# Kernel tuning notes

Hardware: AMD Instinct MI355X
Metric: run time of the kernel (lower is better)

## Reference

```python
import jax, jax.numpy as jnp
import numpy as np

ALPHA = 0.5
BETA = 5.0
LOGIT_SCALE = 100.0  # exp(log(100)) -- CLIP's learned logit scale at its clamp value
NUM_CLASSES = 200


def _l2norm(x):
    return x / jnp.linalg.norm(x, axis=-1, keepdims=True)


def setup_inputs() -> dict:
    key = jax.random.key(0)
    k1, k2, k3, k4 = jax.random.split(key, 4)
    img_f = jax.random.normal(k1, (1024, 512), dtype=jnp.float32)
    text_features = jax.random.normal(k2, (200, 512), dtype=jnp.float32)
    keys = jax.random.normal(k3, (50000, 512), dtype=jnp.float32)
    labels = jax.random.randint(k4, (50000,), 0, NUM_CLASSES, dtype=jnp.int64)
    return {"img_f": img_f, "text_features": text_features, "keys": keys, "labels": labels}


def reference(img_f, text_features, keys, labels):
    # encode_image output is L2-normalized in the module; keys were built from
    # normalized image features, text_features are normalized class embeddings.
    q = _l2norm(img_f)            # [B, D]
    t = _l2norm(text_features)    # [C, D]
    k = _l2norm(keys)             # [N, D]

    # CLIP zero-shot branch: scale * q @ t.T -> [B, C]
    z = LOGIT_SCALE * jnp.einsum('bd,cd->bc', q, t)

    # Tip-Adapter cache branch: exp(beta * q @ keys.T) @ one_hot(labels)
    sim = jnp.einsum('bd,nd->bn', q, k)                 # [B, N]
    aff = jnp.exp(BETA * sim)                           # [B, N]
    values = jax.nn.one_hot(labels, NUM_CLASSES, dtype=aff.dtype)  # [N, C]
    c = aff @ values                                    # [B, C]

    return (1.0 - ALPHA) * z + ALPHA * c
```

## Files before the change

kernel.cpp:

```cpp
#include <hip/hip_runtime.h>

#define B_Q    1024
#define D_K    512
#define N_CLS  200
#define N_KEYS 50000
#define N_PAD  50048
#define N_ZT   (N_PAD / 128)

#define R0 N_PAD
#define R1 (R0 + B_Q)
#define R2 (R1 + N_CLS)
#define R3 (R2 + 56)
#define R4 (R3 + 400)

typedef __attribute__((ext_vector_type(8))) short bf16x8;
typedef __attribute__((ext_vector_type(4))) float f32x4;

__device__ __forceinline__ unsigned short f2bf(float f) {
  union { float f; unsigned int i; } v; v.f = f;
  unsigned int r = v.i + 0x7fffu + ((v.i >> 16) & 1u);
  return (unsigned short)(r >> 16);
}
__device__ __forceinline__ uint4 pack8(const float f[8], float s) {
  uint4 o;
  o.x = (unsigned)f2bf(f[0]*s) | ((unsigned)f2bf(f[1]*s) << 16);
  o.y = (unsigned)f2bf(f[2]*s) | ((unsigned)f2bf(f[3]*s) << 16);
  o.z = (unsigned)f2bf(f[4]*s) | ((unsigned)f2bf(f[5]*s) << 16);
  o.w = (unsigned)f2bf(f[6]*s) | ((unsigned)f2bf(f[7]*s) << 16);
  return o;
}
__device__ __forceinline__ void async_copy16(const void* g, void* lds) {
  __builtin_amdgcn_global_load_lds(
      (const __attribute__((address_space(1))) unsigned int*)g,
      (__attribute__((address_space(3))) unsigned int*)lds, 16, 0, 0);
}

__global__ __launch_bounds__(1024) void k_sort(const int* __restrict__ labels,
                                               int* __restrict__ dest) {
  __shared__ int hist[N_CLS];
  __shared__ int incl[N_CLS];
  __shared__ int cur[N_CLS];
  int t = threadIdx.x;
  if (t < N_CLS) hist[t] = 0;
  __syncthreads();
  for (int n = t; n < N_KEYS; n += 1024) atomicAdd(&hist[labels[n]], 1);
  __syncthreads();
  if (t < N_CLS) incl[t] = hist[t];
  __syncthreads();
  for (int d = 1; d < N_CLS; d <<= 1) {
    int x = 0;
    if (t < N_CLS && t >= d) x = incl[t - d];
    __syncthreads();
    if (t < N_CLS) incl[t] += x;
    __syncthreads();
  }
  if (t < N_CLS) cur[t] = incl[t] - hist[t];
  __syncthreads();
  for (int n = t; n < N_KEYS; n += 1024)
    dest[n] = atomicAdd(&cur[labels[n]], 1);
}

__global__ void k_prep2(const float* __restrict__ keys, const float* __restrict__ img,
                        const float* __restrict__ txt, const int* __restrict__ labels,
                        const int* __restrict__ dest, unsigned short* __restrict__ qn,
                        unsigned short* __restrict__ kn, int* __restrict__ cls,
                        float* __restrict__ out) {
  int w = threadIdx.x >> 6, lane = threadIdx.x & 63;
  int row = blockIdx.x * 4 + w;
  const float* src; unsigned short* dst;
  if (row < R0) {
    if (row >= N_KEYS) {
      *((uint4*)(kn + (size_t)row * D_K) + lane) = make_uint4(0, 0, 0, 0);
      if (lane == 0) cls[row] = N_CLS;
      return;
    }
    int d = dest[row];
    if (lane == 0) cls[d] = labels[row];
    src = keys + (size_t)row * D_K;
    dst = kn + (size_t)d * D_K;
  } else if (row < R1) {
    int r = row - R0;
    src = img + (size_t)r * D_K;
    dst = qn + (size_t)r * D_K;
  } else if (row < R2) {
    int r = row - R1;
    if (lane == 0) cls[N_PAD + r] = N_CLS;
    src = txt + (size_t)r * D_K;
    dst = kn + (size_t)(N_PAD + r) * D_K;
  } else if (row < R3) {
    int r = N_PAD + N_CLS + (row - R2);
    *((uint4*)(kn + (size_t)r * D_K) + lane) = make_uint4(0, 0, 0, 0);
    if (lane == 0) cls[r] = N_CLS;
    return;
  } else if (row < R4) {
    int zr = row - R3;
    uint4* o4 = (uint4*)(out + (size_t)zr * 512) + lane * 2;
    o4[0] = make_uint4(0, 0, 0, 0);
    o4[1] = make_uint4(0, 0, 0, 0);
    return;
  } else return;
  const float4* s4 = (const float4*)src + lane * 2;
  float4 a = s4[0], b = s4[1];
  float f[8] = {a.x, a.y, a.z, a.w, b.x, b.y, b.z, b.w};
  float ss = 0.f;
#pragma unroll
  for (int i = 0; i < 8; i++) ss += f[i] * f[i];
#pragma unroll
  for (int d = 1; d < 64; d <<= 1) ss += __shfl_xor(ss, d);
  float rinv = rsqrtf(ss);
  *((uint4*)dst + lane) = pack8(f, rinv);
}

__global__ __launch_bounds__(256, 3) void k_main(const unsigned short* __restrict__ qn,
                                                 const unsigned short* __restrict__ kn,
                                                 const int* __restrict__ cls,
                                                 float* __restrict__ out) {
  __shared__ unsigned short As[128 * 64];
  __shared__ unsigned short Bs[128 * 64];
  int t = threadIdx.x;
  int tileB = blockIdx.x, tileN = blockIdx.y;
  int rowB0 = tileB * 128, rowN0 = tileN * 128;

  f32x4 acc[4][4];
#pragma unroll
  for (int i = 0; i < 4; i++)
#pragma unroll
    for (int j = 0; j < 4; j++) acc[i][j] = (f32x4){0.f, 0.f, 0.f, 0.f};

  int lane = t & 63, w = t >> 6;
  int wr = (w >> 1) * 64, wc = (w & 1) * 64;
  int l15 = lane & 15, lq = lane >> 4;
  const int rA = t >> 3;
  const int gsw = ((t & 7) ^ (rA & 7)) * 8;
  const int sw = l15 & 7;

  int cj[4];
#pragma unroll
  for (int j = 0; j < 4; j++) cj[j] = cls[rowN0 + wc + 16 * j + l15];
  int cseg0 = cls[rowN0 + wc];
  int cseg1 = cls[rowN0 + wc + 63];

  for (int k0 = 0; k0 < D_K; k0 += 64) {
    __syncthreads();
#pragma unroll
    for (int i = 0; i < 4; i++) {
      int row = i * 32 + rA;
      async_copy16(qn + (size_t)(rowB0 + row) * D_K + k0 + gsw, &As[i * 2048 + t * 8]);
      async_copy16(kn + (size_t)(rowN0 + row) * D_K + k0 + gsw, &Bs[i * 2048 + t * 8]);
    }
    __syncthreads();
#pragma unroll
    for (int ks = 0; ks < 64; ks += 32) {
      bf16x8 af[4], bf[4];
#pragma unroll
      for (int i = 0; i < 4; i++)
        af[i] = *(const bf16x8*)&As[(wr + 16 * i + l15) * 64 + ((((ks >> 3) + lq) ^ sw) * 8)];
#pragma unroll
      for (int j = 0; j < 4; j++)
        bf[j] = *(const bf16x8*)&Bs[(wc + 16 * j + l15) * 64 + ((((ks >> 3) + lq) ^ sw) * 8)];
#pragma unroll
      for (int i = 0; i < 4; i++)
#pragma unroll
        for (int j = 0; j < 4; j++)
          acc[i][j] = __builtin_amdgcn_mfma_f32_16x16x32_bf16(af[i], bf[j], acc[i][j], 0, 0, 0);
    }
  }

  if (tileN >= N_ZT) {
#pragma unroll
    for (int i = 0; i < 4; i++)
#pragma unroll
      for (int j = 0; j < 4; j++) {
        int col = rowN0 + wc + 16 * j + l15 - N_PAD;
        if (col < N_CLS) {
#pragma unroll
          for (int r = 0; r < 4; r++) {
            int row = rowB0 + wr + 16 * i + lq * 4 + r;
            atomicAdd(out + (size_t)row * N_CLS + col, 50.0f * acc[i][j][r]);
          }
        }
      }
    return;
  }

#pragma unroll
  for (int i = 0; i < 4; i++)
#pragma unroll
    for (int j = 0; j < 4; j++)
#pragma unroll
      for (int r = 0; r < 4; r++) acc[i][j][r] = __expf(5.0f * acc[i][j][r]);

  for (int c = cseg0; c <= cseg1; c++) {
    if (c >= N_CLS) break;
#pragma unroll
    for (int i = 0; i < 4; i++) {
      float s0 = 0.f, s1 = 0.f, s2 = 0.f, s3 = 0.f;
#pragma unroll
      for (int j = 0; j < 4; j++) {
        if (cj[j] == c) {
          s0 += acc[i][j][0]; s1 += acc[i][j][1];
          s2 += acc[i][j][2]; s3 += acc[i][j][3];
        }
      }
#pragma unroll
      for (int d = 1; d < 16; d <<= 1) {
        s0 += __shfl_xor(s0, d); s1 += __shfl_xor(s1, d);
        s2 += __shfl_xor(s2, d); s3 += __shfl_xor(s3, d);
      }
      if (l15 == 0) {
        int row = rowB0 + wr + 16 * i + lq * 4;
        float* o = out + (size_t)row * N_CLS + c;
        if (s0 != 0.f) atomicAdd(o + 0 * N_CLS, 0.5f * s0);
        if (s1 != 0.f) atomicAdd(o + 1 * N_CLS, 0.5f * s1);
        if (s2 != 0.f) atomicAdd(o + 2 * N_CLS, 0.5f * s2);
        if (s3 != 0.f) atomicAdd(o + 3 * N_CLS, 0.5f * s3);
      }
    }
  }
}

extern "C" void kernel_launch(void* const* d_in, const int* in_sizes, int n_in,
                              void* d_out, int out_size, void* d_ws, size_t ws_size,
                              hipStream_t stream) {
  (void)in_sizes; (void)n_in; (void)out_size; (void)ws_size;
  const float* img    = (const float*)d_in[0];
  const float* txt    = (const float*)d_in[1];
  const float* keys   = (const float*)d_in[2];
  const int*   labels = (const int*)d_in[3];
  float*       out    = (float*)d_out;

  char* ws = (char*)d_ws;
  unsigned short* qn = (unsigned short*)(ws + 0);
  unsigned short* kn = (unsigned short*)(ws + 1048576);
  int*  dest = (int*)(ws + 52559872);
  int*  cls  = (int*)(ws + 52760064);

  k_sort<<<1, 1024, 0, stream>>>(labels, dest);
  k_prep2<<<(R4 + 3) / 4, 256, 0, stream>>>(keys, img, txt, labels, dest, qn, kn, cls, out);
  k_main<<<dim3(B_Q / 128, N_ZT + 2), 256, 0, stream>>>(qn, kn, cls, out);
}
```

Baseline: 293.8 us.

## Replace single-block label sort with parallel rank and gather via permutation

```diff
diff --git a/kernel.cpp b/kernel.cpp
--- a/kernel.cpp
+++ b/kernel.cpp
@@ -6,6 +6,8 @@
 #define N_KEYS 50000
 #define N_PAD  50048
 #define N_ZT   (N_PAD / 128)
+#define NT_TOT (N_ZT + 2)
+#define KN_ROWS 50304
 
 #define R0 N_PAD
 #define R1 (R0 + B_Q)
@@ -35,17 +37,17 @@
       (__attribute__((address_space(3))) unsigned int*)lds, 16, 0, 0);
 }
 
-__global__ __launch_bounds__(1024) void k_sort(const int* __restrict__ labels,
-                                               int* __restrict__ dest) {
-  __shared__ int hist[N_CLS];
+__global__ void k_zero(int* __restrict__ g) { g[threadIdx.x] = 0; }
+
+__global__ __launch_bounds__(256) void k_rank(const int* __restrict__ labels,
+                                              const int* __restrict__ ghist,
+                                              int* __restrict__ gcnt,
+                                              int* __restrict__ perm,
+                                              int* __restrict__ cls) {
   __shared__ int incl[N_CLS];
-  __shared__ int cur[N_CLS];
+  __shared__ int histl[N_CLS];
   int t = threadIdx.x;
-  if (t < N_CLS) hist[t] = 0;
-  __syncthreads();
-  for (int n = t; n < N_KEYS; n += 1024) atomicAdd(&hist[labels[n]], 1);
-  __syncthreads();
-  if (t < N_CLS) incl[t] = hist[t];
+  if (t < N_CLS) { int h = ghist[t]; histl[t] = h; incl[t] = h; }
   __syncthreads();
   for (int d = 1; d < N_CLS; d <<= 1) {
     int x = 0;
@@ -54,43 +56,45 @@
     if (t < N_CLS) incl[t] += x;
     __syncthreads();
   }
-  if (t < N_CLS) cur[t] = incl[t] - hist[t];
-  __syncthreads();
-  for (int n = t; n < N_KEYS; n += 1024)
-    dest[n] = atomicAdd(&cur[labels[n]], 1);
+  int n = blockIdx.x * 256 + t;
+  if (n < N_KEYS) {
+    int lab = labels[n];
+    int r = atomicAdd(&gcnt[lab], 1);
+    int d = incl[lab] - histl[lab] + r;
+    perm[d] = n;
+    cls[d] = lab;
+  } else if (n < KN_ROWS) {
+    perm[n] = n;
+    cls[n] = N_CLS;
+  }
 }
 
 __global__ void k_prep2(const float* __restrict__ keys, const float* __restrict__ img,
                         const float* __restrict__ txt, const int* __restrict__ labels,
-                        const int* __restrict__ dest, unsigned short* __restrict__ qn,
-                        unsigned short* __restrict__ kn, int* __restrict__ cls,
-                        float* __restrict__ out) {
+                        unsigned short* __restrict__ qn, unsigned short* __restrict__ kn,
+                        int* __restrict__ ghist, float* __restrict__ out) {
   int w = threadIdx.x >> 6, lane = threadIdx.x & 63;
   int row = blockIdx.x * 4 + w;
   const float* src; unsigned short* dst;
   if (row < R0) {
     if (row >= N_KEYS) {
       *((uint4*)(kn + (size_t)row * D_K) + lane) = make_uint4(0, 0, 0, 0);
-      if (lane == 0) cls[row] = N_CLS;
       return;
     }
-    int d = dest[row];
-    if (lane == 0) cls[d] = labels[row];
+    if (lane == 0) atomicAdd(&ghist[labels[row]], 1);
     src = keys + (size_t)row * D_K;
-    dst = kn + (size_t)d * D_K;
+    dst = kn + (size_t)row * D_K;
   } else if (row < R1) {
     int r = row - R0;
     src = img + (size_t)r * D_K;
     dst = qn + (size_t)r * D_K;
   } else if (row < R2) {
     int r = row - R1;
-    if (lane == 0) cls[N_PAD + r] = N_CLS;
     src = txt + (size_t)r * D_K;
     dst = kn + (size_t)(N_PAD + r) * D_K;
   } else if (row < R3) {
     int r = N_PAD + N_CLS + (row - R2);
     *((uint4*)(kn + (size_t)r * D_K) + lane) = make_uint4(0, 0, 0, 0);
-    if (lane == 0) cls[r] = N_CLS;
     return;
   } else if (row < R4) {
     int zr = row - R3;
@@ -111,14 +115,16 @@
   *((uint4*)dst + lane) = pack8(f, rinv);
 }
 
-__global__ __launch_bounds__(256, 3) void k_main(const unsigned short* __restrict__ qn,
+__global__ __launch_bounds__(256, 5) void k_main(const unsigned short* __restrict__ qn,
                                                  const unsigned short* __restrict__ kn,
                                                  const int* __restrict__ cls,
+                                                 const int* __restrict__ perm,
                                                  float* __restrict__ out) {
   __shared__ unsigned short As[128 * 64];
   __shared__ unsigned short Bs[128 * 64];
   int t = threadIdx.x;
-  int tileB = blockIdx.x, tileN = blockIdx.y;
+  int wsw = (blockIdx.x & 7) * NT_TOT + (blockIdx.x >> 3);
+  int tileN = wsw >> 3, tileB = wsw & 7;
   int rowB0 = tileB * 128, rowN0 = tileN * 128;
 
   f32x4 acc[4][4];
@@ -134,6 +140,9 @@
   const int gsw = ((t & 7) ^ (rA & 7)) * 8;
   const int sw = l15 & 7;
 
+  int prow[4];
+#pragma unroll
+  for (int i = 0; i < 4; i++) prow[i] = perm[rowN0 + i * 32 + rA];
   int cj[4];
 #pragma unroll
   for (int j = 0; j < 4; j++) cj[j] = cls[rowN0 + wc + 16 * j + l15];
@@ -146,7 +155,7 @@
     for (int i = 0; i < 4; i++) {
       int row = i * 32 + rA;
       async_copy16(qn + (size_t)(rowB0 + row) * D_K + k0 + gsw, &As[i * 2048 + t * 8]);
-      async_copy16(kn + (size_t)(rowN0 + row) * D_K + k0 + gsw, &Bs[i * 2048 + t * 8]);
+      async_copy16(kn + (size_t)prow[i] * D_K + k0 + gsw, &Bs[i * 2048 + t * 8]);
     }
     __syncthreads();
 #pragma unroll
@@ -232,10 +241,12 @@
   char* ws = (char*)d_ws;
   unsigned short* qn = (unsigned short*)(ws + 0);
   unsigned short* kn = (unsigned short*)(ws + 1048576);
-  int*  dest = (int*)(ws + 52559872);
-  int*  cls  = (int*)(ws + 52760064);
-
-  k_sort<<<1, 1024, 0, stream>>>(labels, dest);
-  k_prep2<<<(R4 + 3) / 4, 256, 0, stream>>>(keys, img, txt, labels, dest, qn, kn, cls, out);
-  k_main<<<dim3(B_Q / 128, N_ZT + 2), 256, 0, stream>>>(qn, kn, cls, out);
-}
+  int*  perm = (int*)(ws + 52559872);
+  int*  cls  = (int*)(ws + 52761088);
+  int*  gz   = (int*)(ws + 52962304);
+
+  k_zero<<<1, 512, 0, stream>>>(gz);
+  k_prep2<<<(R4 + 3) / 4, 256, 0, stream>>>(keys, img, txt, labels, qn, kn, gz, out);
+  k_rank<<<(KN_ROWS + 255) / 256, 256, 0, stream>>>(labels, gz, gz + 256, perm, cls);
+  k_main<<<dim3(8 * NT_TOT), 256, 0, stream>>>(qn, kn, cls, perm, out);
+}
```

After: 434.9 us. 1.48x slower.
